# Performance work log

Measured on AMD Instinct MI355X. Metric: run time of the kernel, lower is better.

Reference implementation:

```python
import jax, jax.numpy as jnp
import numpy as np

_GAUSS_2D = np.array([[1.,4.,6.,4.,1.],[4.,16.,24.,16.,4.],[6.,24.,36.,24.,6.],[4.,16.,24.,16.,4.],[1.,4.,6.,4.,1.]], dtype=np.float32) / 256.0
_GX = np.array([[2.,0.,-2.],[4.,0.,-4.],[2.,0.,-2.]], dtype=np.float32)
_GY = np.array([[2.,4.,2.],[0.,0.,0.],[-2.,-4.,-2.]], dtype=np.float32)


def _conv_gauss(img, kernel):
    # reflect-pad by 2 on H,W (matches F.pad(img,(2,2,2,2),'reflect')), then depthwise VALID conv
    img = jnp.pad(img, ((0, 0), (0, 0), (2, 2), (2, 2)), mode='reflect')
    return jax.lax.conv_general_dilated(
        img, kernel, window_strides=(1, 1), padding='VALID',
        feature_group_count=img.shape[1],
        dimension_numbers=('NCHW', 'OIHW', 'NCHW'))


def _downsample(x):
    return x[:, :, ::2, ::2]


def _upsample(x, gk):
    # zero-interleave: x at even (h,w) indices, zeros elsewhere, then smooth with 4*gauss
    B, C, H, W = x.shape
    up = jnp.zeros((B, C, 2 * H, 2 * W), dtype=x.dtype).at[:, :, ::2, ::2].set(x)
    return _conv_gauss(up, 4.0 * gk)


def _laplacian_pyramid(img, gk, max_levels=3):
    C = img.shape[1]
    gx = jnp.broadcast_to(jnp.asarray(_GX)[None, None], (C, 1, 3, 3))
    gy = jnp.broadcast_to(jnp.asarray(_GY)[None, None], (C, 1, 3, 3))
    current = img
    pyr = []
    for _ in range(max_levels):
        filtered = _conv_gauss(current, gk)
        down = _downsample(filtered)
        up = _upsample(down, gk)
        diff = current - up
        # note: pad=2 with 3x3 kernel -> output is (H+2, W+2), faithful to source
        miniloss = jnp.abs(_conv_gauss(diff, gx)) + jnp.abs(_conv_gauss(diff, gy))
        pyr.append(miniloss)
        current = down
    return pyr


def setup_inputs() -> dict:
    key = jax.random.key(0)
    k1, k2 = jax.random.split(key)
    B, C, H, W = 16, 3, 512, 512
    inp = jax.random.normal(k1, (B, C, H, W), dtype=jnp.float32)
    tgt = jax.random.normal(k2, (B, C, H, W), dtype=jnp.float32)
    gk = jnp.broadcast_to(jnp.asarray(_GAUSS_2D)[None, None], (C, 1, 5, 5)).astype(jnp.float32)
    return {'input': inp, 'target': tgt, 'gauss_kernel': gk}


def reference(input, target, gauss_kernel):
    max_levels = 3
    pyr_in = _laplacian_pyramid(input, gauss_kernel, max_levels)
    pyr_tg = _laplacian_pyramid(target, gauss_kernel, max_levels)
    loss = jnp.asarray(0.0, dtype=input.dtype)
    for a, b in zip(pyr_in, pyr_tg):
        loss = loss + jnp.mean(jnp.abs(a - b))  # l1_loss, mean reduction
    return loss
```

## Files before the change

### kernel.cpp

```cpp
#include <hip/hip_runtime.h>


#define NCH 48

__device__ __forceinline__ int refl(int p, int n) {
  return p < 0 ? -p : (p >= n ? 2 * n - 2 - p : p);
}
__device__ __forceinline__ int dref(int j, int n) {
  return j < 0 ? -j : (j >= n ? 2 * n - 1 - j : j);
}

__global__ __launch_bounds__(256) void down_kernel(
    const float* __restrict__ src_a, const float* __restrict__ src_b,
    float* __restrict__ dst_a, float* __restrict__ dst_b, int H)
{
  const int W = H, W2 = W >> 1;
  const int bx = blockIdx.x, by = blockIdx.y;
  const int z = blockIdx.z;
  const int ch = (z >= NCH) ? z - NCH : z;
  const float* src = ((z >= NCH) ? src_b : src_a) + (size_t)ch * H * W;
  float* dst = ((z >= NCH) ? dst_b : dst_a) + (size_t)ch * W2 * W2;
  const int tid = threadIdx.x;

  __shared__ __align__(16) float s_h[67][34];

  const int rb = 64 * by - 2;
  const int C0 = 64 * bx - 4;
  const bool lft = (bx == 0);
  const bool rgt = (64 * bx + 64 >= W);

  for (int t = tid; t < 67 * 18; t += 256) {
    int r = t / 18, c4 = t - 18 * r;
    int gr = refl(rb + r, H);
    int gb = min(max(C0 + 4 * c4, 0), W - 4);
    float4 v = *reinterpret_cast<const float4*>(src + (size_t)gr * W + gb);
    float pz = __shfl_up(v.z, 1);
    float pw = __shfl_up(v.w, 1);
    float nx = __shfl_down(v.x, 1);
    if (c4 >= 1 && c4 <= 16) {
      float hb0;
      if (lft && c4 == 1)
        hb0 = v.z + 4.f * v.y + 6.f * v.x + 4.f * v.y + v.z;
      else
        hb0 = pz + 4.f * pw + 6.f * v.x + 4.f * v.y + v.z;
      float nxe = (rgt && c4 == 16) ? v.z : nx;
      float hb1 = v.x + 4.f * v.y + 6.f * v.z + 4.f * v.w + nxe;
      *reinterpret_cast<float2*>(&s_h[r][2 * c4 - 2]) = make_float2(hb0, hb1);
    }
  }
  __syncthreads();

  {
    int r = tid >> 3, g = tid & 7;
    float4 h0 = *reinterpret_cast<const float4*>(&s_h[2 * r][4 * g]);
    float4 h1 = *reinterpret_cast<const float4*>(&s_h[2 * r + 1][4 * g]);
    float4 h2 = *reinterpret_cast<const float4*>(&s_h[2 * r + 2][4 * g]);
    float4 h3 = *reinterpret_cast<const float4*>(&s_h[2 * r + 3][4 * g]);
    float4 h4 = *reinterpret_cast<const float4*>(&s_h[2 * r + 4][4 * g]);
    float4 o;
    o.x = (h0.x + h4.x + 6.f * h2.x + 4.f * (h1.x + h3.x)) * (1.f / 256.f);
    o.y = (h0.y + h4.y + 6.f * h2.y + 4.f * (h1.y + h3.y)) * (1.f / 256.f);
    o.z = (h0.z + h4.z + 6.f * h2.z + 4.f * (h1.z + h3.z)) * (1.f / 256.f);
    o.w = (h0.w + h4.w + 6.f * h2.w + 4.f * (h1.w + h3.w)) * (1.f / 256.f);
    *reinterpret_cast<float4*>(dst + (size_t)(32 * by + r) * W2 + 32 * bx + 4 * g) = o;
  }
}

__global__ __launch_bounds__(256) void loss_kernel(
    const float* __restrict__ in, const float* __restrict__ tg,
    const float* __restrict__ d0i, const float* __restrict__ d0t,
    const float* __restrict__ d1i, const float* __restrict__ d1t,
    const float* __restrict__ d2i, const float* __restrict__ d2t,
    double* __restrict__ partials)
{
  int tb = blockIdx.x;
  int lvl, bx, by;
  if (tb < 289) { lvl = 0; by = tb / 17; bx = tb - 17 * by; }
  else if (tb < 370) { int u = tb - 289; lvl = 1; by = u / 9; bx = u - 9 * by; }
  else { int u = tb - 370; lvl = 2; by = u / 5; bx = u - 5 * by; }

  const int H = 512 >> lvl, W = H, HO = H + 2, H2 = H >> 1, W2 = W >> 1;
  const int n = blockIdx.z;
  const float* cb0 = (lvl == 0) ? in : (lvl == 1) ? d0i : d1i;
  const float* cb1 = (lvl == 0) ? tg : (lvl == 1) ? d0t : d1t;
  const float* db0 = (lvl == 0) ? d0i : (lvl == 1) ? d1i : d2i;
  const float* db1 = (lvl == 0) ? d0t : (lvl == 1) ? d1t : d2t;
  const float* curp[2] = {cb0 + (size_t)n * H * W, cb1 + (size_t)n * H * W};
  const float* dwp[2] = {db0 + (size_t)n * H2 * W2, db1 + (size_t)n * H2 * W2};
  const float scale = 1.f / (float)(NCH * HO * HO);

  const int x0 = bx * 32, y0 = by * 32;
  const int tid = threadIdx.x;

  __shared__ __align__(16) float s_diff[2][36][52];
  __shared__ __align__(16) float s_tmp[2][36][24];
  __shared__ __align__(16) float s_down[2][20][24];

  const int cbase = x0 - 8, rbase = y0 - 2;
  const int dr0 = (y0 >> 1) - 2, du0 = (x0 >> 1) - 4;
  const bool vec = (x0 >= 32) && (x0 + 40 <= W);
  const int x_end = min(HO, x0 + 32), y_end = min(HO, y0 + 32);

  if (vec) {
    for (int t = tid; t < 864; t += 256) {
      int img = t >= 432; int j = t - (img ? 432 : 0);
      int l = j / 12, c4 = j - 12 * l;
      int gr = refl(rbase + l, H);
      *reinterpret_cast<float4*>(&s_diff[img][l][4 * c4]) =
          *reinterpret_cast<const float4*>(curp[img] + (size_t)gr * W + cbase + 4 * c4);
    }
    if (tid < 240) {
      int img = tid >= 120; int j = tid - (img ? 120 : 0);
      int k = j / 6, c4 = j - 6 * k;
      int gr = dref(dr0 + k, H2);
      *reinterpret_cast<float4*>(&s_down[img][k][4 * c4]) =
          *reinterpret_cast<const float4*>(dwp[img] + (size_t)gr * W2 + du0 + 4 * c4);
    }
  } else {
    for (int t = tid; t < 3456; t += 256) {
      int img = t >= 1728; int j = t - (img ? 1728 : 0);
      int l = j / 48, c = j - 48 * l;
      int gr = refl(rbase + l, H), gc = refl(cbase + c, W);
      s_diff[img][l][c] = curp[img][(size_t)gr * W + gc];
    }
    for (int t = tid; t < 960; t += 256) {
      int img = t >= 480; int j = t - (img ? 480 : 0);
      int k = j / 24, c = j - 24 * k;
      int gr = dref(dr0 + k, H2), gc = dref(du0 + c, W2);
      s_down[img][k][c] = dwp[img][(size_t)gr * W2 + gc];
    }
  }
  __syncthreads();

  for (int t = tid; t < 432; t += 256) {
    int img = t / 216, j = t - 216 * img;
    int l = j / 6, c4 = j - 6 * l;
    int rr = (l + (l & 1)) >> 1;
    float4 a = *reinterpret_cast<const float4*>(&s_down[img][rr][4 * c4]);
    float4 b = *reinterpret_cast<const float4*>(&s_down[img][rr + 1][4 * c4]);
    float4 o;
    if (l & 1) {
      o.x = 0.5f * (a.x + b.x);
      o.y = 0.5f * (a.y + b.y);
      o.z = 0.5f * (a.z + b.z);
      o.w = 0.5f * (a.w + b.w);
    } else {
      float4 cc = *reinterpret_cast<const float4*>(&s_down[img][rr + 2][4 * c4]);
      o.x = 0.125f * (a.x + cc.x) + 0.75f * b.x;
      o.y = 0.125f * (a.y + cc.y) + 0.75f * b.y;
      o.z = 0.125f * (a.z + cc.z) + 0.75f * b.z;
      o.w = 0.125f * (a.w + cc.w) + 0.75f * b.w;
    }
    *reinterpret_cast<float4*>(&s_tmp[img][l][4 * c4]) = o;
  }
  __syncthreads();

  for (int t = tid; t < 720; t += 256) {
    int img = t / 360, j = t - 360 * img;
    int l = j / 10, c4 = j - 10 * l;
    float4 c = *reinterpret_cast<const float4*>(&s_diff[img][l][4 * c4 + 4]);
    const float* st = s_tmp[img][l];
    float Tm1 = st[2 * c4 + 1], T0 = st[2 * c4 + 2], T1 = st[2 * c4 + 3], T2 = st[2 * c4 + 4];
    float4 d;
    d.x = c.x - (0.125f * (Tm1 + T1) + 0.75f * T0);
    d.y = c.y - 0.5f * (T0 + T1);
    d.z = c.z - (0.125f * (T0 + T2) + 0.75f * T1);
    d.w = c.w - 0.5f * (T1 + T2);
    *reinterpret_cast<float4*>(&s_diff[img][l][4 * c4 + 4]) = d;
  }
  __syncthreads();

  float val = 0.f;
  {
    const int tx = tid & 7, ty = tid >> 3;
    const int yy = y0 + ty;
    if (yy < y_end) {
      float ab[2][4];
#pragma unroll
      for (int img = 0; img < 2; ++img) {
        float a[3][6];
#pragma unroll
        for (int r = 0; r < 3; ++r) {
          const float* row = s_diff[img][ty + r];
          float2 L = *reinterpret_cast<const float2*>(&row[4 * tx + 6]);
          float4 R = *reinterpret_cast<const float4*>(&row[4 * tx + 8]);
          a[r][0] = L.x; a[r][1] = L.y; a[r][2] = R.x;
          a[r][3] = R.y; a[r][4] = R.z; a[r][5] = R.w;
        }
        float s[6], d[6], v[6];
#pragma unroll
        for (int k = 0; k < 6; ++k) {
          s[k] = a[0][k] + a[2][k];
          d[k] = a[0][k] - a[2][k];
          v[k] = 2.f * s[k] + 4.f * a[1][k];
        }
#pragma unroll
        for (int jj = 0; jj < 4; ++jj) {
          float gx = v[jj] - v[jj + 2];
          float u  = (d[jj] + d[jj + 2]) + 2.f * d[jj + 1];
          ab[img][jj] = fabsf(gx) + 2.f * fabsf(u);
        }
      }
      const int xb = x0 + 4 * tx;
#pragma unroll
      for (int jj = 0; jj < 4; ++jj)
        if (xb + jj < x_end) val += fabsf(ab[0][jj] - ab[1][jj]);
    }
  }
  val *= scale;

#pragma unroll
  for (int off = 32; off > 0; off >>= 1) val += __shfl_down(val, off, 64);
  __shared__ float wpart[4];
  if ((tid & 63) == 0) wpart[tid >> 6] = val;
  __syncthreads();
  if (tid == 0) {
    double s = (double)wpart[0] + (double)wpart[1] + (double)wpart[2] + (double)wpart[3];
    partials[blockIdx.z * 395 + blockIdx.x] = s;
  }
}

__global__ __launch_bounds__(1024) void finalize_kernel(
    const double* __restrict__ partials, int N, float* __restrict__ out)
{
  double s = 0.0;
  for (int i = threadIdx.x; i < N; i += 1024) s += partials[i];
#pragma unroll
  for (int off = 32; off > 0; off >>= 1)
    s += __shfl_down(s, off, 64);
  __shared__ double wp[16];
  if ((threadIdx.x & 63) == 0) wp[threadIdx.x >> 6] = s;
  __syncthreads();
  if (threadIdx.x == 0) {
    double t = 0.0;
#pragma unroll
    for (int i = 0; i < 16; ++i) t += wp[i];
    out[0] = (float)t;
  }
}

extern "C" void kernel_launch(void* const* d_in, const int* in_sizes, int n_in,
                              void* d_out, int out_size, void* d_ws, size_t ws_size,
                              hipStream_t stream) {
  const float* in = (const float*)d_in[0];
  const float* tg = (const float*)d_in[1];
  float* out = (float*)d_out;

  const int NPART = 18960;
  double* partials = (double*)d_ws;
  float* base = (float*)((char*)d_ws + (size_t)NPART * sizeof(double));
  const size_t s0 = (size_t)NCH * 256 * 256;
  const size_t s1 = (size_t)NCH * 128 * 128;
  float* d0i = base;
  float* d0t = d0i + s0;
  float* d1i = d0t + s0;
  float* d1t = d1i + s1;
  float* d2i = d1t + s1;
  float* d2t = d2i + (size_t)NCH * 64 * 64;

  down_kernel<<<dim3(8, 8, 2 * NCH), dim3(256), 0, stream>>>(in, tg, d0i, d0t, 512);
  down_kernel<<<dim3(4, 4, 2 * NCH), dim3(256), 0, stream>>>(d0i, d0t, d1i, d1t, 256);
  down_kernel<<<dim3(2, 2, 2 * NCH), dim3(256), 0, stream>>>(d1i, d1t, d2i, d2t, 128);

  loss_kernel<<<dim3(395, 1, NCH), dim3(256), 0, stream>>>(
      in, tg, d0i, d0t, d1i, d1t, d2i, d2t, partials);

  finalize_kernel<<<1, dim3(1024), 0, stream>>>(partials, NPART, out);
}
```

Measured before the change: 256.6 us.

## Swizzle block order across XCDs and vectorize edge-tile loads

```diff
diff --git a/kernel.cpp b/kernel.cpp
--- a/kernel.cpp
+++ b/kernel.cpp
@@ -12,11 +12,17 @@
 
 __global__ __launch_bounds__(256) void down_kernel(
     const float* __restrict__ src_a, const float* __restrict__ src_b,
-    float* __restrict__ dst_a, float* __restrict__ dst_b, int H)
+    float* __restrict__ dst_a, float* __restrict__ dst_b, int H, int tl)
 {
   const int W = H, W2 = W >> 1;
-  const int bx = blockIdx.x, by = blockIdx.y;
-  const int z = blockIdx.z;
+  const int tps = 1 << tl, nt = tps * tps;
+  const int total = 96 * nt;
+  const int bid = blockIdx.x;
+  const int s = (bid & 7) * (total >> 3) + (bid >> 3);
+  const int z = s >> (2 * tl);
+  const int rm = s & (nt - 1);
+  const int by = rm >> tl, bx = rm & (tps - 1);
+
   const int ch = (z >= NCH) ? z - NCH : z;
   const float* src = ((z >= NCH) ? src_b : src_a) + (size_t)ch * H * W;
   float* dst = ((z >= NCH) ? dst_b : dst_a) + (size_t)ch * W2 * W2;
@@ -73,20 +79,22 @@
     const float* __restrict__ d2i, const float* __restrict__ d2t,
     double* __restrict__ partials)
 {
-  int tb = blockIdx.x;
+  const int bid = blockIdx.x;
+  const int swz = (bid & 7) * 2370 + (bid >> 3);
+  const int z = swz / 395;
+  int tb = swz - 395 * z;
   int lvl, bx, by;
   if (tb < 289) { lvl = 0; by = tb / 17; bx = tb - 17 * by; }
   else if (tb < 370) { int u = tb - 289; lvl = 1; by = u / 9; bx = u - 9 * by; }
   else { int u = tb - 370; lvl = 2; by = u / 5; bx = u - 5 * by; }
 
   const int H = 512 >> lvl, W = H, HO = H + 2, H2 = H >> 1, W2 = W >> 1;
-  const int n = blockIdx.z;
   const float* cb0 = (lvl == 0) ? in : (lvl == 1) ? d0i : d1i;
   const float* cb1 = (lvl == 0) ? tg : (lvl == 1) ? d0t : d1t;
   const float* db0 = (lvl == 0) ? d0i : (lvl == 1) ? d1i : d2i;
   const float* db1 = (lvl == 0) ? d0t : (lvl == 1) ? d1t : d2t;
-  const float* curp[2] = {cb0 + (size_t)n * H * W, cb1 + (size_t)n * H * W};
-  const float* dwp[2] = {db0 + (size_t)n * H2 * W2, db1 + (size_t)n * H2 * W2};
+  const float* curp[2] = {cb0 + (size_t)z * H * W, cb1 + (size_t)z * H * W};
+  const float* dwp[2] = {db0 + (size_t)z * H2 * W2, db1 + (size_t)z * H2 * W2};
   const float scale = 1.f / (float)(NCH * HO * HO);
 
   const int x0 = bx * 32, y0 = by * 32;
@@ -117,17 +125,39 @@
           *reinterpret_cast<const float4*>(dwp[img] + (size_t)gr * W2 + du0 + 4 * c4);
     }
   } else {
-    for (int t = tid; t < 3456; t += 256) {
-      int img = t >= 1728; int j = t - (img ? 1728 : 0);
-      int l = j / 48, c = j - 48 * l;
-      int gr = refl(rbase + l, H), gc = refl(cbase + c, W);
-      s_diff[img][l][c] = curp[img][(size_t)gr * W + gc];
-    }
-    for (int t = tid; t < 960; t += 256) {
-      int img = t >= 480; int j = t - (img ? 480 : 0);
-      int k = j / 24, c = j - 24 * k;
-      int gr = dref(dr0 + k, H2), gc = dref(du0 + c, W2);
-      s_down[img][k][c] = dwp[img][(size_t)gr * W2 + gc];
+    for (int t = tid; t < 864; t += 256) {
+      int img = t >= 432; int j = t - (img ? 432 : 0);
+      int l = j / 12, g = j - 12 * l;
+      int gr = refl(rbase + l, H);
+      const float* rowp = curp[img] + (size_t)gr * W;
+      int p0 = cbase + 4 * g;
+      float4 v;
+      if (p0 >= 0 && p0 + 3 < W) {
+        v = *reinterpret_cast<const float4*>(rowp + p0);
+      } else {
+        v.x = rowp[refl(p0, W)];
+        v.y = rowp[refl(p0 + 1, W)];
+        v.z = rowp[refl(p0 + 2, W)];
+        v.w = rowp[refl(p0 + 3, W)];
+      }
+      *reinterpret_cast<float4*>(&s_diff[img][l][4 * g]) = v;
+    }
+    if (tid < 240) {
+      int img = tid >= 120; int j = tid - (img ? 120 : 0);
+      int k = j / 6, g = j - 6 * k;
+      int gr = dref(dr0 + k, H2);
+      const float* rowp = dwp[img] + (size_t)gr * W2;
+      int p0 = du0 + 4 * g;
+      float4 v;
+      if (p0 >= 0 && p0 + 3 < W2) {
+        v = *reinterpret_cast<const float4*>(rowp + p0);
+      } else {
+        v.x = rowp[dref(p0, W2)];
+        v.y = rowp[dref(p0 + 1, W2)];
+        v.z = rowp[dref(p0 + 2, W2)];
+        v.w = rowp[dref(p0 + 3, W2)];
+      }
+      *reinterpret_cast<float4*>(&s_down[img][k][4 * g]) = v;
     }
   }
   __syncthreads();
@@ -160,7 +190,10 @@
     int l = j / 10, c4 = j - 10 * l;
     float4 c = *reinterpret_cast<const float4*>(&s_diff[img][l][4 * c4 + 4]);
     const float* st = s_tmp[img][l];
-    float Tm1 = st[2 * c4 + 1], T0 = st[2 * c4 + 2], T1 = st[2 * c4 + 3], T2 = st[2 * c4 + 4];
+    float2 A2 = *reinterpret_cast<const float2*>(&st[2 * c4]);
+    float2 B2 = *reinterpret_cast<const float2*>(&st[2 * c4 + 2]);
+    float T2 = st[2 * c4 + 4];
+    float Tm1 = A2.y, T0 = B2.x, T1 = B2.y;
     float4 d;
     d.x = c.x - (0.125f * (Tm1 + T1) + 0.75f * T0);
     d.y = c.y - 0.5f * (T0 + T1);
@@ -216,7 +249,7 @@
   __syncthreads();
   if (tid == 0) {
     double s = (double)wpart[0] + (double)wpart[1] + (double)wpart[2] + (double)wpart[3];
-    partials[blockIdx.z * 395 + blockIdx.x] = s;
+    partials[swz] = s;
   }
 }
 
@@ -258,11 +291,11 @@
   float* d2i = d1t + s1;
   float* d2t = d2i + (size_t)NCH * 64 * 64;
 
-  down_kernel<<<dim3(8, 8, 2 * NCH), dim3(256), 0, stream>>>(in, tg, d0i, d0t, 512);
-  down_kernel<<<dim3(4, 4, 2 * NCH), dim3(256), 0, stream>>>(d0i, d0t, d1i, d1t, 256);
-  down_kernel<<<dim3(2, 2, 2 * NCH), dim3(256), 0, stream>>>(d1i, d1t, d2i, d2t, 128);
-
-  loss_kernel<<<dim3(395, 1, NCH), dim3(256), 0, stream>>>(
+  down_kernel<<<dim3(6144), dim3(256), 0, stream>>>(in, tg, d0i, d0t, 512, 3);
+  down_kernel<<<dim3(1536), dim3(256), 0, stream>>>(d0i, d0t, d1i, d1t, 256, 2);
+  down_kernel<<<dim3(384), dim3(256), 0, stream>>>(d1i, d1t, d2i, d2t, 128, 1);
+
+  loss_kernel<<<dim3(18960), dim3(256), 0, stream>>>(
       in, tg, d0i, d0t, d1i, d1t, d2i, d2t, partials);
 
   finalize_kernel<<<1, dim3(1024), 0, stream>>>(partials, NPART, out);
```

Measured after the change: 231.0 us. -10.0%, faster.
